# Kernel tuning notes

Hardware: AMD Instinct MI355X
Metric: run time of the kernel (lower is better)

## Reference

```python
import jax, jax.numpy as jnp
import numpy as np

N = 8192
IN, HID, NH, TOT = 64, 64, 4, 128
DH = TOT // NH  # 32


def setup_inputs() -> dict:
    key = jax.random.key(0)
    ks = jax.random.split(key, 8)
    s = 0.05
    return {
        "input": jax.random.normal(ks[0], (N, IN), jnp.float32),
        "hx": jax.random.normal(ks[1], (N, HID), jnp.float32),
        "Wq": jax.random.normal(ks[2], (NH, TOT, DH), jnp.float32) * s,
        "Wk": jax.random.normal(ks[3], (NH, TOT, DH), jnp.float32) * s,
        "Wr": jax.random.normal(ks[4], (TOT, HID), jnp.float32) * s,
        "br": jnp.zeros((HID,), jnp.float32),
        "Wz": jax.random.normal(ks[5], (TOT, HID), jnp.float32) * s,
        "bz": jnp.zeros((HID,), jnp.float32),
        "Wh": jax.random.normal(ks[6], (TOT, HID), jnp.float32) * s,
        "bh": jnp.zeros((HID,), jnp.float32),
    }


def _dyn_adj(x, Wq, Wk):
    # x: [N, T]; multi-head attention adjacency, averaged over heads -> [N, N]
    q = jnp.einsum('nt,htd->hnd', x, Wq)
    k = jnp.einsum('nt,htd->hnd', x, Wk)
    scores = jnp.einsum('hnd,hmd->hnm', q, k) / jnp.sqrt(jnp.float32(DH))
    return jnp.mean(jax.nn.softmax(scores, axis=-1), axis=0)  # [N, N]


def reference(input, hx, Wq, Wk, Wr, br, Wz, bz, Wh, bh):
    x = jnp.concatenate([input, hx], axis=1)          # [N, TOT]
    adj = _dyn_adj(x, Wq, Wk)                         # [N, N] row-stochastic
    ax = adj @ x                                      # shared adjacency application
    r = jax.nn.sigmoid(ax @ Wr + br)                  # [N, HID]
    z = jax.nn.sigmoid(ax @ Wz + bz)                  # [N, HID]
    x2 = jnp.concatenate([input, r * hx], axis=1)     # [N, TOT]
    h = jnp.tanh((adj @ x2) @ Wh + bh)                # [N, HID]
    return z * hx + (1.0 - z) * h
```

## Files before the change

### kernel.cpp

```cpp
#include <hip/hip_runtime.h>
#include <hip/hip_bf16.h>

#define NN 8192
#define TOTD 128
#define HIDD 64
#define NHEAD 4
#define DHD 32
#define NCQ 16
#define JPB (NN / 32 / NCQ)

typedef __attribute__((ext_vector_type(8))) short short8;
typedef __attribute__((ext_vector_type(4))) float f32x4;
typedef __attribute__((ext_vector_type(16))) float f32x16;

__device__ __forceinline__ short f2b(float f) {
  unsigned u = __builtin_bit_cast(unsigned, f);
  u += 0x7fff + ((u >> 16) & 1);
  return (short)(u >> 16);
}
__device__ __forceinline__ short f2b_fast(float f) {
  unsigned u = __builtin_bit_cast(unsigned, f);
  return (short)((u + 0x8000u) >> 16);
}
__device__ __forceinline__ float fexp2(float x) {
#if __has_builtin(__builtin_amdgcn_exp2f)
  return __builtin_amdgcn_exp2f(x);
#else
  return exp2f(x);
#endif
}
__device__ __forceinline__ f32x16 zero16() {
  f32x16 z;
#pragma unroll
  for (int i = 0; i < 16; ++i) z[i] = 0.f;
  return z;
}


__global__ void k_build_xfrag(const float* __restrict__ in, const float* __restrict__ hx,
                              short* __restrict__ xb) {
  int i = blockIdx.x * 256 + threadIdx.x;
  int n = i >> 7;
  int t = i & 127;
  float v = (t < 64) ? in[n * 64 + t] : hx[n * 64 + (t - 64)];
  int jt = n >> 5, nn = n & 31;
  int m = nn >> 4, rem = nn & 15;
  int hi = (rem >> 2) & 1;
  int e = (rem & 3) | ((rem >> 3) << 2);
  int ct = t >> 5;
  int lane = (hi << 5) | (t & 31);
  xb[(((size_t)jt * 8 + ct * 2 + m) << 9) + (lane << 3) + e] = f2b(v);
}

__global__ __launch_bounds__(256, 2) void k_qk(
    const float* __restrict__ in, const float* __restrict__ hx,
    const float* __restrict__ Wq, const float* __restrict__ Wk,
    short* __restrict__ qb, short* __restrict__ kb) {
  __shared__ float Ws[32 * 256];
  __shared__ float xr_t[128 * 16];
  const int tid = threadIdx.x;
  const int n0 = blockIdx.x * 16;
  for (int i = tid; i < 2048; i += 256) {
    int r = i & 15, t = i >> 4;
    xr_t[t * 16 + r] = (t < 64) ? in[(n0 + r) * 64 + t] : hx[(n0 + r) * 64 + (t - 64)];
  }
  const int which = tid >> 7;
  const int h = (tid >> 5) & 3;
  const int d = tid & 31;
  const int c = tid;
  float acc[16];
#pragma unroll
  for (int r = 0; r < 16; ++r) acc[r] = 0.f;

  for (int pass = 0; pass < 4; ++pass) {
    __syncthreads();
    for (int i = tid; i < 32 * 256; i += 256) {
      int tt = pass * 32 + (i >> 8);
      int cc = i & 255;
      const float* W = (cc < 128) ? Wq : Wk;
      int hh = (cc >> 5) & 3, dd = cc & 31;
      Ws[(i >> 8) * 256 + cc] = W[((size_t)hh * 128 + tt) * 32 + dd];
    }
    __syncthreads();
#pragma unroll
    for (int t = 0; t < 32; ++t) {
      float wv = Ws[t * 256 + c];
      const float4* xp = (const float4*)&xr_t[(pass * 32 + t) * 16];
      float4 x0 = xp[0], x1 = xp[1], x2 = xp[2], x3 = xp[3];
      acc[0] += x0.x * wv;  acc[1] += x0.y * wv;  acc[2] += x0.z * wv;  acc[3] += x0.w * wv;
      acc[4] += x1.x * wv;  acc[5] += x1.y * wv;  acc[6] += x1.z * wv;  acc[7] += x1.w * wv;
      acc[8] += x2.x * wv;  acc[9] += x2.y * wv;  acc[10] += x2.z * wv; acc[11] += x2.w * wv;
      acc[12] += x3.x * wv; acc[13] += x3.y * wv; acc[14] += x3.z * wv; acc[15] += x3.w * wv;
    }
  }
#pragma unroll
  for (int r = 0; r < 16; ++r) {
    int n = n0 + r;
    int lane = (((d >> 3) & 1) << 5) | (n & 31);
    size_t idx = ((((size_t)(n >> 5) * 4 + h) * 2 + (d >> 4)) << 9) + (lane << 3) + (d & 7);
    if (which == 0) qb[idx] = f2b(acc[r] * 0.25503486f);
    else            kb[idx] = f2b(acc[r]);
  }
}

__global__ __launch_bounds__(256, 4) void k_denom(
    const short* __restrict__ qb, const short* __restrict__ kb,
    float* __restrict__ lpart_g) {
  const int tid = threadIdx.x;
  const int w = tid >> 6, l = tid & 63;
  const int r0 = blockIdx.x * 128 + w * 32;
  const int rt = blockIdx.x * 4 + w;
  const int jt0 = blockIdx.y * JPB;

  short8 qf[NHEAD][2];
#pragma unroll
  for (int h = 0; h < NHEAD; ++h)
#pragma unroll
    for (int m = 0; m < 2; ++m)
      qf[h][m] = *(const short8*)&qb[((((size_t)rt * 4 + h) * 2 + m) << 9) + l * 8];

  float acc[NHEAD] = {0.f, 0.f, 0.f, 0.f};

  for (int j = 0; j < JPB; ++j) {
    const short* kbase = kb + (((size_t)(jt0 + j) * 8) << 9) + l * 8;
#pragma unroll
    for (int h = 0; h < NHEAD; ++h) {
      short8 kf0 = *(const short8*)&kbase[(h * 2 + 0) << 9];
      short8 kf1 = *(const short8*)&kbase[(h * 2 + 1) << 9];
      f32x16 s = __builtin_amdgcn_mfma_f32_32x32x16_bf16(kf0, qf[h][0], zero16(), 0, 0, 0);
      s = __builtin_amdgcn_mfma_f32_32x32x16_bf16(kf1, qf[h][1], s, 0, 0, 0);
#pragma unroll
      for (int r = 0; r < 16; ++r) acc[h] += fexp2(s[r]);
    }
  }
#pragma unroll
  for (int h = 0; h < NHEAD; ++h) acc[h] += __shfl_xor(acc[h], 32, 64);
  if (l < 32) {
#pragma unroll
    for (int h = 0; h < NHEAD; ++h)
      lpart_g[((size_t)blockIdx.y * NHEAD + h) * NN + r0 + l] = acc[h];
  }
}

__global__ void k_linv(const float* __restrict__ lpart_g, float* __restrict__ linv_g) {
  int i = blockIdx.x * 256 + threadIdx.x;
  float s = 0.f;
#pragma unroll
  for (int q = 0; q < NCQ; ++q) s += lpart_g[(size_t)q * NHEAD * NN + i];
  linv_g[i] = 0.25f / s;
}

__global__ __launch_bounds__(256, 2) void k_pv1(
    const short* __restrict__ qb, const short* __restrict__ kb,
    const short* __restrict__ xb, const float* __restrict__ linv_g,
    float* __restrict__ axq) {
  const int tid = threadIdx.x;
  const int w = tid >> 6, l = tid & 63;
  const int hi = l >> 5, col = l & 31;
  const int r0 = blockIdx.x * 128 + w * 32;
  const int rt = blockIdx.x * 4 + w;
  const int jt0 = blockIdx.y * JPB;

  short8 qf[NHEAD][2];
#pragma unroll
  for (int h = 0; h < NHEAD; ++h)
#pragma unroll
    for (int m = 0; m < 2; ++m)
      qf[h][m] = *(const short8*)&qb[((((size_t)rt * 4 + h) * 2 + m) << 9) + l * 8];
  float linv[NHEAD];
#pragma unroll
  for (int h = 0; h < NHEAD; ++h) linv[h] = linv_g[h * NN + r0 + col];

  f32x16 axa[4];
#pragma unroll
  for (int ct = 0; ct < 4; ++ct) axa[ct] = zero16();

  for (int j = 0; j < JPB; ++j) {
    const size_t jt = jt0 + j;
    const short* kbase = kb + ((jt * 8) << 9) + l * 8;
    const short* xbase = xb + ((jt * 8) << 9) + l * 8;
    short8 xv[8];
#pragma unroll
    for (int cchunk = 0; cchunk < 8; ++cchunk)
      xv[cchunk] = *(const short8*)&xbase[cchunk << 9];
    float p[16];
#pragma unroll
    for (int r = 0; r < 16; ++r) p[r] = 0.f;
#pragma unroll
    for (int h = 0; h < NHEAD; ++h) {
      short8 kf0 = *(const short8*)&kbase[(h * 2 + 0) << 9];
      short8 kf1 = *(const short8*)&kbase[(h * 2 + 1) << 9];
      f32x16 s = __builtin_amdgcn_mfma_f32_32x32x16_bf16(kf0, qf[h][0], zero16(), 0, 0, 0);
      s = __builtin_amdgcn_mfma_f32_32x32x16_bf16(kf1, qf[h][1], s, 0, 0, 0);
#pragma unroll
      for (int r = 0; r < 16; ++r) p[r] += fexp2(s[r]) * linv[h];
    }
    short8 pa0, pa1;
#pragma unroll
    for (int e = 0; e < 8; ++e) { pa0[e] = f2b_fast(p[e]); pa1[e] = f2b_fast(p[8 + e]); }
#pragma unroll
    for (int ct = 0; ct < 4; ++ct) {
      axa[ct] = __builtin_amdgcn_mfma_f32_32x32x16_bf16(pa0, xv[ct * 2 + 0], axa[ct], 0, 0, 0);
      axa[ct] = __builtin_amdgcn_mfma_f32_32x32x16_bf16(pa1, xv[ct * 2 + 1], axa[ct], 0, 0, 0);
    }
  }
#pragma unroll
  for (int ct = 0; ct < 4; ++ct)
#pragma unroll
    for (int r = 0; r < 16; ++r) {
      int row = (r & 3) + 8 * (r >> 2) + 4 * hi;
      axq[(size_t)blockIdx.y * NN * TOTD + (size_t)(r0 + row) * TOTD + ct * 32 + col] =
          axa[ct][r];
    }
}

__global__ void k_rz(const float* __restrict__ axq, const float* __restrict__ hx,
                     const float* __restrict__ Wr, const float* __restrict__ br,
                     const float* __restrict__ Wz, const float* __restrict__ bz,
                     float* __restrict__ ax, float* __restrict__ z,
                     short* __restrict__ v2f) {
  __shared__ float axs[2][TOTD];
  int tid = threadIdx.x;
  int rr = tid >> 7;
  int c2 = tid & 127;
  int n = blockIdx.x * 2 + rr;
  float s = 0.f;
#pragma unroll
  for (int q = 0; q < NCQ; ++q) s += axq[(size_t)q * NN * TOTD + (size_t)n * TOTD + c2];
  axs[rr][c2] = s;
  ax[(size_t)n * TOTD + c2] = s;
  __syncthreads();
  bool isz = c2 >= HIDD;
  int c = c2 & (HIDD - 1);
  const float* W = isz ? Wz : Wr;
  float acc = isz ? bz[c] : br[c];
#pragma unroll
  for (int t = 0; t < TOTD; ++t) acc += axs[rr][t] * W[t * HIDD + c];
  float sg = 1.f / (1.f + __expf(-acc));
  if (isz) {
    z[n * HIDD + c] = sg;
  } else {
    int jt = n >> 5, nn = n & 31;
    int m = nn >> 4, rem = nn & 15;
    int hi = (rem >> 2) & 1;
    int e = (rem & 3) | ((rem >> 3) << 2);
    int ct = c >> 5;
    int lane = (hi << 5) | (c & 31);
    v2f[(((size_t)jt * 4 + ct * 2 + m) << 9) + (lane << 3) + e] = f2b(sg * hx[n * HIDD + c]);
  }
}

__global__ __launch_bounds__(256, 3) void k_pv2(
    const short* __restrict__ qb, const short* __restrict__ kb,
    const short* __restrict__ v2f, const float* __restrict__ linv_g,
    float* __restrict__ a2q) {
  const int tid = threadIdx.x;
  const int w = tid >> 6, l = tid & 63;
  const int hi = l >> 5, col = l & 31;
  const int r0 = blockIdx.x * 128 + w * 32;
  const int rt = blockIdx.x * 4 + w;
  const int jt0 = blockIdx.y * JPB;

  short8 qf[NHEAD][2];
#pragma unroll
  for (int h = 0; h < NHEAD; ++h)
#pragma unroll
    for (int m = 0; m < 2; ++m)
      qf[h][m] = *(const short8*)&qb[((((size_t)rt * 4 + h) * 2 + m) << 9) + l * 8];
  float linv[NHEAD];
#pragma unroll
  for (int h = 0; h < NHEAD; ++h) linv[h] = linv_g[h * NN + r0 + col];

  f32x16 a2a[2];
#pragma unroll
  for (int ct = 0; ct < 2; ++ct) a2a[ct] = zero16();

  for (int j = 0; j < JPB; ++j) {
    const size_t jt = jt0 + j;
    const short* kbase = kb + ((jt * 8) << 9) + l * 8;
    const short* vbase = v2f + ((jt * 4) << 9) + l * 8;
    short8 vv[4];
#pragma unroll
    for (int cchunk = 0; cchunk < 4; ++cchunk)
      vv[cchunk] = *(const short8*)&vbase[cchunk << 9];
    float p[16];
#pragma unroll
    for (int r = 0; r < 16; ++r) p[r] = 0.f;
#pragma unroll
    for (int h = 0; h < NHEAD; ++h) {
      short8 kf0 = *(const short8*)&kbase[(h * 2 + 0) << 9];
      short8 kf1 = *(const short8*)&kbase[(h * 2 + 1) << 9];
      f32x16 s = __builtin_amdgcn_mfma_f32_32x32x16_bf16(kf0, qf[h][0], zero16(), 0, 0, 0);
      s = __builtin_amdgcn_mfma_f32_32x32x16_bf16(kf1, qf[h][1], s, 0, 0, 0);
#pragma unroll
      for (int r = 0; r < 16; ++r) p[r] += fexp2(s[r]) * linv[h];
    }
    short8 pa0, pa1;
#pragma unroll
    for (int e = 0; e < 8; ++e) { pa0[e] = f2b_fast(p[e]); pa1[e] = f2b_fast(p[8 + e]); }
#pragma unroll
    for (int ct = 0; ct < 2; ++ct) {
      a2a[ct] = __builtin_amdgcn_mfma_f32_32x32x16_bf16(pa0, vv[ct * 2 + 0], a2a[ct], 0, 0, 0);
      a2a[ct] = __builtin_amdgcn_mfma_f32_32x32x16_bf16(pa1, vv[ct * 2 + 1], a2a[ct], 0, 0, 0);
    }
  }
#pragma unroll
  for (int ct = 0; ct < 2; ++ct)
#pragma unroll
    for (int r = 0; r < 16; ++r) {
      int row = (r & 3) + 8 * (r >> 2) + 4 * hi;
      a2q[(size_t)blockIdx.y * NN * HIDD + (size_t)(r0 + row) * HIDD + ct * 32 + col] =
          a2a[ct][r];
    }
}

__global__ __launch_bounds__(256) void k_final(
    const float* __restrict__ a2q, const float* __restrict__ ax,
    const float* __restrict__ hx, const float* __restrict__ Wh,
    const float* __restrict__ bh, const float* __restrict__ z,
    float* __restrict__ out) {
  __shared__ float Whs[TOTD * HIDD];
  __shared__ float a2s[16][HIDD];
  const int tid = threadIdx.x;
  const int r0 = blockIdx.x * 16;

  for (int i = tid; i < TOTD * HIDD; i += 256) Whs[i] = Wh[i];
  for (int i = tid; i < 16 * HIDD; i += 256) {
    int rw = i >> 6, c = i & 63;
    size_t gi = (size_t)(r0 + rw) * HIDD + c;
    float s = 0.f;
#pragma unroll
    for (int q = 0; q < NCQ; ++q) s += a2q[(size_t)q * NN * HIDD + gi];
    a2s[rw][c] = s;
  }
  __syncthreads();
  for (int o = tid; o < 16 * HIDD; o += 256) {
    int rw = o >> 6, c = o & 63;
    const float* axrow = &ax[(size_t)(r0 + rw) * TOTD];
    float acc = bh[c];
#pragma unroll
    for (int t = 0; t < 64; ++t) acc += axrow[t] * Whs[t * HIDD + c];
#pragma unroll
    for (int t = 0; t < 64; ++t) acc += a2s[rw][t] * Whs[(64 + t) * HIDD + c];
    float hval = tanhf(acc);
    size_t gi = (size_t)(r0 + rw) * HIDD + c;
    float zz = z[gi];
    out[gi] = zz * hx[gi] + (1.f - zz) * hval;
  }
}

extern "C" void kernel_launch(void* const* d_in, const int* in_sizes, int n_in,
                              void* d_out, int out_size, void* d_ws, size_t ws_size,
                              hipStream_t stream) {
  const float* in = (const float*)d_in[0];
  const float* hx = (const float*)d_in[1];
  const float* Wq = (const float*)d_in[2];
  const float* Wk = (const float*)d_in[3];
  const float* Wr = (const float*)d_in[4];
  const float* br = (const float*)d_in[5];
  const float* Wz = (const float*)d_in[6];
  const float* bz = (const float*)d_in[7];
  const float* Wh = (const float*)d_in[8];
  const float* bh = (const float*)d_in[9];

  const size_t MB = 1ull << 20;
  char* ws = (char*)d_ws;
  short* qb    = (short*)(ws + 0 * MB);
  short* kb    = (short*)(ws + 2 * MB);
  short* xb    = (short*)(ws + 4 * MB);
  float* linv  = (float*)(ws + 6 * MB);
  float* lpart = (float*)(ws + 7 * MB);
  float* ax    = (float*)(ws + 10 * MB);
  float* z     = (float*)(ws + 14 * MB);
  short* v2f   = (short*)(ws + 16 * MB);
  float* axq   = (float*)(ws + 20 * MB);
  float* a2q   = (float*)(ws + 84 * MB);
  float* out   = (float*)d_out;

  k_build_xfrag<<<dim3((NN * TOTD) / 256), dim3(256), 0, stream>>>(in, hx, xb);
  k_qk<<<dim3(NN / 16), dim3(256), 0, stream>>>(in, hx, Wq, Wk, qb, kb);
  k_denom<<<dim3(NN / 128, NCQ), dim3(256), 0, stream>>>(qb, kb, lpart);
  k_linv<<<dim3((NHEAD * NN) / 256), dim3(256), 0, stream>>>(lpart, linv);
  k_pv1<<<dim3(NN / 128, NCQ), dim3(256), 0, stream>>>(qb, kb, xb, linv, axq);
  k_rz<<<dim3(NN / 2), dim3(256), 0, stream>>>(axq, hx, Wr, br, Wz, bz, ax, z, v2f);
  k_pv2<<<dim3(NN / 128, NCQ), dim3(256), 0, stream>>>(qb, kb, v2f, linv, a2q);
  k_final<<<dim3(NN / 16), dim3(256), 0, stream>>>(a2q, ax, hx, Wh, bh, z, out);
}
```

Before: 210.0 us.

## Stage K/X/V tiles through LDS with async double buffering; store partials in bf16

The three attention kernels now copy each key tile (and X or V tile) into a double-buffered shared-memory array with global_load_lds, prefetching the next tile while the current one is consumed. Each wave issues part of the copy, replacing per-wave redundant global loads. The split-K partial sums axq and a2q are written in bf16 instead of fp32, halving that traffic. k_rz now handles 8 rows per block so weight loads are reused, and ax keeps only the 64 columns k_final reads. Occupancy hints are raised. The costs are a block-wide barrier every tile, extra LDS per block, and bf16 rounding on partials before the 16-way reduction.

```diff
diff --git a/kernel.cpp b/kernel.cpp
--- a/kernel.cpp
+++ b/kernel.cpp
@@ -22,6 +22,10 @@
   unsigned u = __builtin_bit_cast(unsigned, f);
   return (short)((u + 0x8000u) >> 16);
 }
+__device__ __forceinline__ float b2f(short s) {
+  unsigned u = ((unsigned)(unsigned short)s) << 16;
+  return __builtin_bit_cast(float, u);
+}
 __device__ __forceinline__ float fexp2(float x) {
 #if __has_builtin(__builtin_amdgcn_exp2f)
   return __builtin_amdgcn_exp2f(x);
@@ -34,6 +38,11 @@
 #pragma unroll
   for (int i = 0; i < 16; ++i) z[i] = 0.f;
   return z;
+}
+__device__ __forceinline__ void gl_lds16(const short* g, short* l) {
+  __builtin_amdgcn_global_load_lds(
+      (const __attribute__((address_space(1))) void*)g,
+      (__attribute__((address_space(3))) void*)l, 16, 0, 0);
 }
 
 
@@ -103,9 +112,10 @@
   }
 }
 
-__global__ __launch_bounds__(256, 4) void k_denom(
+__global__ __launch_bounds__(256, 6) void k_denom(
     const short* __restrict__ qb, const short* __restrict__ kb,
     float* __restrict__ lpart_g) {
+  __shared__ short kbuf[2][8 * 512];
   const int tid = threadIdx.x;
   const int w = tid >> 6, l = tid & 63;
   const int r0 = blockIdx.x * 128 + w * 32;
@@ -121,17 +131,29 @@
 
   float acc[NHEAD] = {0.f, 0.f, 0.f, 0.f};
 
+#pragma unroll
+  for (int c = w * 2; c < w * 2 + 2; ++c)
+    gl_lds16(kb + (((size_t)jt0 * 8 + c) << 9) + l * 8, &kbuf[0][c * 512]);
+  __syncthreads();
+
   for (int j = 0; j < JPB; ++j) {
-    const short* kbase = kb + (((size_t)(jt0 + j) * 8) << 9) + l * 8;
+    int b = j & 1;
+    if (j + 1 < JPB) {
+#pragma unroll
+      for (int c = w * 2; c < w * 2 + 2; ++c)
+        gl_lds16(kb + (((size_t)(jt0 + j + 1) * 8 + c) << 9) + l * 8, &kbuf[b ^ 1][c * 512]);
+    }
+    const short* cur = kbuf[b];
 #pragma unroll
     for (int h = 0; h < NHEAD; ++h) {
-      short8 kf0 = *(const short8*)&kbase[(h * 2 + 0) << 9];
-      short8 kf1 = *(const short8*)&kbase[(h * 2 + 1) << 9];
+      short8 kf0 = *(const short8*)&cur[(h * 2 + 0) * 512 + l * 8];
+      short8 kf1 = *(const short8*)&cur[(h * 2 + 1) * 512 + l * 8];
       f32x16 s = __builtin_amdgcn_mfma_f32_32x32x16_bf16(kf0, qf[h][0], zero16(), 0, 0, 0);
       s = __builtin_amdgcn_mfma_f32_32x32x16_bf16(kf1, qf[h][1], s, 0, 0, 0);
 #pragma unroll
       for (int r = 0; r < 16; ++r) acc[h] += fexp2(s[r]);
     }
+    __syncthreads();
   }
 #pragma unroll
   for (int h = 0; h < NHEAD; ++h) acc[h] += __shfl_xor(acc[h], 32, 64);
@@ -150,10 +172,11 @@
   linv_g[i] = 0.25f / s;
 }
 
-__global__ __launch_bounds__(256, 2) void k_pv1(
+__global__ __launch_bounds__(256, 3) void k_pv1(
     const short* __restrict__ qb, const short* __restrict__ kb,
     const short* __restrict__ xb, const float* __restrict__ linv_g,
-    float* __restrict__ axq) {
+    short* __restrict__ axq) {
+  __shared__ short kx[2][16 * 512];
   const int tid = threadIdx.x;
   const int w = tid >> 6, l = tid & 63;
   const int hi = l >> 5, col = l & 31;
@@ -175,21 +198,32 @@
 #pragma unroll
   for (int ct = 0; ct < 4; ++ct) axa[ct] = zero16();
 
+#pragma unroll
+  for (int c = w * 4; c < w * 4 + 4; ++c) {
+    const short* src = (c < 8) ? kb + (((size_t)jt0 * 8 + c) << 9) + l * 8
+                               : xb + (((size_t)jt0 * 8 + (c - 8)) << 9) + l * 8;
+    gl_lds16(src, &kx[0][c * 512]);
+  }
+  __syncthreads();
+
   for (int j = 0; j < JPB; ++j) {
-    const size_t jt = jt0 + j;
-    const short* kbase = kb + ((jt * 8) << 9) + l * 8;
-    const short* xbase = xb + ((jt * 8) << 9) + l * 8;
-    short8 xv[8];
-#pragma unroll
-    for (int cchunk = 0; cchunk < 8; ++cchunk)
-      xv[cchunk] = *(const short8*)&xbase[cchunk << 9];
+    int b = j & 1;
+    if (j + 1 < JPB) {
+#pragma unroll
+      for (int c = w * 4; c < w * 4 + 4; ++c) {
+        const short* src = (c < 8) ? kb + (((size_t)(jt0 + j + 1) * 8 + c) << 9) + l * 8
+                                   : xb + (((size_t)(jt0 + j + 1) * 8 + (c - 8)) << 9) + l * 8;
+        gl_lds16(src, &kx[b ^ 1][c * 512]);
+      }
+    }
+    const short* cur = kx[b];
     float p[16];
 #pragma unroll
     for (int r = 0; r < 16; ++r) p[r] = 0.f;
 #pragma unroll
     for (int h = 0; h < NHEAD; ++h) {
-      short8 kf0 = *(const short8*)&kbase[(h * 2 + 0) << 9];
-      short8 kf1 = *(const short8*)&kbase[(h * 2 + 1) << 9];
+      short8 kf0 = *(const short8*)&cur[(h * 2 + 0) * 512 + l * 8];
+      short8 kf1 = *(const short8*)&cur[(h * 2 + 1) * 512 + l * 8];
       f32x16 s = __builtin_amdgcn_mfma_f32_32x32x16_bf16(kf0, qf[h][0], zero16(), 0, 0, 0);
       s = __builtin_amdgcn_mfma_f32_32x32x16_bf16(kf1, qf[h][1], s, 0, 0, 0);
 #pragma unroll
@@ -200,9 +234,12 @@
     for (int e = 0; e < 8; ++e) { pa0[e] = f2b_fast(p[e]); pa1[e] = f2b_fast(p[8 + e]); }
 #pragma unroll
     for (int ct = 0; ct < 4; ++ct) {
-      axa[ct] = __builtin_amdgcn_mfma_f32_32x32x16_bf16(pa0, xv[ct * 2 + 0], axa[ct], 0, 0, 0);
-      axa[ct] = __builtin_amdgcn_mfma_f32_32x32x16_bf16(pa1, xv[ct * 2 + 1], axa[ct], 0, 0, 0);
-    }
+      short8 xv0 = *(const short8*)&cur[(8 + ct * 2 + 0) * 512 + l * 8];
+      short8 xv1 = *(const short8*)&cur[(8 + ct * 2 + 1) * 512 + l * 8];
+      axa[ct] = __builtin_amdgcn_mfma_f32_32x32x16_bf16(pa0, xv0, axa[ct], 0, 0, 0);
+      axa[ct] = __builtin_amdgcn_mfma_f32_32x32x16_bf16(pa1, xv1, axa[ct], 0, 0, 0);
+    }
+    __syncthreads();
   }
 #pragma unroll
   for (int ct = 0; ct < 4; ++ct)
@@ -210,50 +247,67 @@
     for (int r = 0; r < 16; ++r) {
       int row = (r & 3) + 8 * (r >> 2) + 4 * hi;
       axq[(size_t)blockIdx.y * NN * TOTD + (size_t)(r0 + row) * TOTD + ct * 32 + col] =
-          axa[ct][r];
-    }
-}
-
-__global__ void k_rz(const float* __restrict__ axq, const float* __restrict__ hx,
-                     const float* __restrict__ Wr, const float* __restrict__ br,
-                     const float* __restrict__ Wz, const float* __restrict__ bz,
-                     float* __restrict__ ax, float* __restrict__ z,
-                     short* __restrict__ v2f) {
-  __shared__ float axs[2][TOTD];
-  int tid = threadIdx.x;
-  int rr = tid >> 7;
-  int c2 = tid & 127;
-  int n = blockIdx.x * 2 + rr;
-  float s = 0.f;
-#pragma unroll
-  for (int q = 0; q < NCQ; ++q) s += axq[(size_t)q * NN * TOTD + (size_t)n * TOTD + c2];
-  axs[rr][c2] = s;
-  ax[(size_t)n * TOTD + c2] = s;
+          f2b(axa[ct][r]);
+    }
+}
+
+__global__ __launch_bounds__(256) void k_rz(
+    const short* __restrict__ axq, const float* __restrict__ hx,
+    const float* __restrict__ Wr, const float* __restrict__ br,
+    const float* __restrict__ Wz, const float* __restrict__ bz,
+    float* __restrict__ ax, float* __restrict__ z, short* __restrict__ v2f) {
+  __shared__ float axs[8][TOTD];
+  const int tid = threadIdx.x;
+  const int n0 = blockIdx.x * 8;
+  for (int i = tid; i < 8 * TOTD; i += 256) {
+    int rw = i >> 7, c = i & 127;
+    int n = n0 + rw;
+    float s = 0.f;
+#pragma unroll
+    for (int q = 0; q < NCQ; ++q) s += b2f(axq[((size_t)q * NN + n) * TOTD + c]);
+    axs[rw][c] = s;
+    if (c < 64) ax[(size_t)n * HIDD + c] = s;
+  }
   __syncthreads();
-  bool isz = c2 >= HIDD;
-  int c = c2 & (HIDD - 1);
+  const int c2 = tid & 127;
+  const int half = tid >> 7;
+  const bool isz = c2 >= HIDD;
+  const int c = c2 & (HIDD - 1);
   const float* W = isz ? Wz : Wr;
-  float acc = isz ? bz[c] : br[c];
-#pragma unroll
-  for (int t = 0; t < TOTD; ++t) acc += axs[rr][t] * W[t * HIDD + c];
-  float sg = 1.f / (1.f + __expf(-acc));
-  if (isz) {
-    z[n * HIDD + c] = sg;
-  } else {
-    int jt = n >> 5, nn = n & 31;
-    int m = nn >> 4, rem = nn & 15;
-    int hi = (rem >> 2) & 1;
-    int e = (rem & 3) | ((rem >> 3) << 2);
-    int ct = c >> 5;
-    int lane = (hi << 5) | (c & 31);
-    v2f[(((size_t)jt * 4 + ct * 2 + m) << 9) + (lane << 3) + e] = f2b(sg * hx[n * HIDD + c]);
-  }
-}
-
-__global__ __launch_bounds__(256, 3) void k_pv2(
+  const float bias = isz ? bz[c] : br[c];
+  float a0 = bias, a1 = bias, a2 = bias, a3 = bias;
+#pragma unroll
+  for (int t = 0; t < TOTD; ++t) {
+    float wv = W[t * HIDD + c];
+    a0 += axs[half * 4 + 0][t] * wv;
+    a1 += axs[half * 4 + 1][t] * wv;
+    a2 += axs[half * 4 + 2][t] * wv;
+    a3 += axs[half * 4 + 3][t] * wv;
+  }
+  float accs[4] = {a0, a1, a2, a3};
+#pragma unroll
+  for (int r = 0; r < 4; ++r) {
+    int n = n0 + half * 4 + r;
+    float sg = 1.f / (1.f + __expf(-accs[r]));
+    if (isz) {
+      z[(size_t)n * HIDD + c] = sg;
+    } else {
+      int jt = n >> 5, nn = n & 31;
+      int m = nn >> 4, rem = nn & 15;
+      int hh = (rem >> 2) & 1;
+      int e = (rem & 3) | ((rem >> 3) << 2);
+      int ct = c >> 5;
+      int lane = (hh << 5) | (c & 31);
+      v2f[(((size_t)jt * 4 + ct * 2 + m) << 9) + (lane << 3) + e] = f2b(sg * hx[(size_t)n * HIDD + c]);
+    }
+  }
+}
+
+__global__ __launch_bounds__(256, 4) void k_pv2(
     const short* __restrict__ qb, const short* __restrict__ kb,
     const short* __restrict__ v2f, const float* __restrict__ linv_g,
-    float* __restrict__ a2q) {
+    short* __restrict__ a2q) {
+  __shared__ short kv[2][12 * 512];
   const int tid = threadIdx.x;
   const int w = tid >> 6, l = tid & 63;
   const int hi = l >> 5, col = l & 31;
@@ -275,21 +329,32 @@
 #pragma unroll
   for (int ct = 0; ct < 2; ++ct) a2a[ct] = zero16();
 
+#pragma unroll
+  for (int c = w * 3; c < w * 3 + 3; ++c) {
+    const short* src = (c < 8) ? kb + (((size_t)jt0 * 8 + c) << 9) + l * 8
+                               : v2f + (((size_t)jt0 * 4 + (c - 8)) << 9) + l * 8;
+    gl_lds16(src, &kv[0][c * 512]);
+  }
+  __syncthreads();
+
   for (int j = 0; j < JPB; ++j) {
-    const size_t jt = jt0 + j;
-    const short* kbase = kb + ((jt * 8) << 9) + l * 8;
-    const short* vbase = v2f + ((jt * 4) << 9) + l * 8;
-    short8 vv[4];
-#pragma unroll
-    for (int cchunk = 0; cchunk < 4; ++cchunk)
-      vv[cchunk] = *(const short8*)&vbase[cchunk << 9];
+    int b = j & 1;
+    if (j + 1 < JPB) {
+#pragma unroll
+      for (int c = w * 3; c < w * 3 + 3; ++c) {
+        const short* src = (c < 8) ? kb + (((size_t)(jt0 + j + 1) * 8 + c) << 9) + l * 8
+                                   : v2f + (((size_t)(jt0 + j + 1) * 4 + (c - 8)) << 9) + l * 8;
+        gl_lds16(src, &kv[b ^ 1][c * 512]);
+      }
+    }
+    const short* cur = kv[b];
     float p[16];
 #pragma unroll
     for (int r = 0; r < 16; ++r) p[r] = 0.f;
 #pragma unroll
     for (int h = 0; h < NHEAD; ++h) {
-      short8 kf0 = *(const short8*)&kbase[(h * 2 + 0) << 9];
-      short8 kf1 = *(const short8*)&kbase[(h * 2 + 1) << 9];
+      short8 kf0 = *(const short8*)&cur[(h * 2 + 0) * 512 + l * 8];
+      short8 kf1 = *(const short8*)&cur[(h * 2 + 1) * 512 + l * 8];
       f32x16 s = __builtin_amdgcn_mfma_f32_32x32x16_bf16(kf0, qf[h][0], zero16(), 0, 0, 0);
       s = __builtin_amdgcn_mfma_f32_32x32x16_bf16(kf1, qf[h][1], s, 0, 0, 0);
 #pragma unroll
@@ -300,9 +365,12 @@
     for (int e = 0; e < 8; ++e) { pa0[e] = f2b_fast(p[e]); pa1[e] = f2b_fast(p[8 + e]); }
 #pragma unroll
     for (int ct = 0; ct < 2; ++ct) {
-      a2a[ct] = __builtin_amdgcn_mfma_f32_32x32x16_bf16(pa0, vv[ct * 2 + 0], a2a[ct], 0, 0, 0);
-      a2a[ct] = __builtin_amdgcn_mfma_f32_32x32x16_bf16(pa1, vv[ct * 2 + 1], a2a[ct], 0, 0, 0);
-    }
+      short8 vv0 = *(const short8*)&cur[(8 + ct * 2 + 0) * 512 + l * 8];
+      short8 vv1 = *(const short8*)&cur[(8 + ct * 2 + 1) * 512 + l * 8];
+      a2a[ct] = __builtin_amdgcn_mfma_f32_32x32x16_bf16(pa0, vv0, a2a[ct], 0, 0, 0);
+      a2a[ct] = __builtin_amdgcn_mfma_f32_32x32x16_bf16(pa1, vv1, a2a[ct], 0, 0, 0);
+    }
+    __syncthreads();
   }
 #pragma unroll
   for (int ct = 0; ct < 2; ++ct)
@@ -310,12 +378,12 @@
     for (int r = 0; r < 16; ++r) {
       int row = (r & 3) + 8 * (r >> 2) + 4 * hi;
       a2q[(size_t)blockIdx.y * NN * HIDD + (size_t)(r0 + row) * HIDD + ct * 32 + col] =
-          a2a[ct][r];
+          f2b(a2a[ct][r]);
     }
 }
 
 __global__ __launch_bounds__(256) void k_final(
-    const float* __restrict__ a2q, const float* __restrict__ ax,
+    const short* __restrict__ a2q, const float* __restrict__ ax,
     const float* __restrict__ hx, const float* __restrict__ Wh,
     const float* __restrict__ bh, const float* __restrict__ z,
     float* __restrict__ out) {
@@ -330,13 +398,13 @@
     size_t gi = (size_t)(r0 + rw) * HIDD + c;
     float s = 0.f;
 #pragma unroll
-    for (int q = 0; q < NCQ; ++q) s += a2q[(size_t)q * NN * HIDD + gi];
+    for (int q = 0; q < NCQ; ++q) s += b2f(a2q[(size_t)q * NN * HIDD + gi]);
     a2s[rw][c] = s;
   }
   __syncthreads();
   for (int o = tid; o < 16 * HIDD; o += 256) {
     int rw = o >> 6, c = o & 63;
-    const float* axrow = &ax[(size_t)(r0 + rw) * TOTD];
+    const float* axrow = &ax[(size_t)(r0 + rw) * HIDD];
     float acc = bh[c];
 #pragma unroll
     for (int t = 0; t < 64; ++t) acc += axrow[t] * Whs[t * HIDD + c];
@@ -371,10 +439,10 @@
   float* linv  = (float*)(ws + 6 * MB);
   float* lpart = (float*)(ws + 7 * MB);
   float* ax    = (float*)(ws + 10 * MB);
-  float* z     = (float*)(ws + 14 * MB);
-  short* v2f   = (short*)(ws + 16 * MB);
-  float* axq   = (float*)(ws + 20 * MB);
-  float* a2q   = (float*)(ws + 84 * MB);
+  float* z     = (float*)(ws + 13 * MB);
+  short* v2f   = (short*)(ws + 15 * MB);
+  short* axq   = (short*)(ws + 17 * MB);
+  short* a2q   = (short*)(ws + 50 * MB);
   float* out   = (float*)d_out;
 
   k_build_xfrag<<<dim3((NN * TOTD) / 256), dim3(256), 0, stream>>>(in, hx, xb);
@@ -382,7 +450,7 @@
   k_denom<<<dim3(NN / 128, NCQ), dim3(256), 0, stream>>>(qb, kb, lpart);
   k_linv<<<dim3((NHEAD * NN) / 256), dim3(256), 0, stream>>>(lpart, linv);
   k_pv1<<<dim3(NN / 128, NCQ), dim3(256), 0, stream>>>(qb, kb, xb, linv, axq);
-  k_rz<<<dim3(NN / 2), dim3(256), 0, stream>>>(axq, hx, Wr, br, Wz, bz, ax, z, v2f);
+  k_rz<<<dim3(NN / 8), dim3(256), 0, stream>>>(axq, hx, Wr, br, Wz, bz, ax, z, v2f);
   k_pv2<<<dim3(NN / 128, NCQ), dim3(256), 0, stream>>>(qb, kb, v2f, linv, a2q);
   k_final<<<dim3(NN / 16), dim3(256), 0, stream>>>(a2q, ax, hx, Wh, bh, z, out);
 }
```

Measured after the change: 393.7 us. 1.88x slower.
